# Optimization experiments

Hardware: AMD Instinct MI355X
Metric: run time of the kernel (lower is better)

The kernel has to match this reference:

```python
import jax, jax.numpy as jnp
import numpy as np

N = 100000   # nodes
E = 3200000  # edges
G = 512      # graphs in batch
EPS = 1e-5   # batchnorm eps


def _lin(key, fan_in, fan_out):
    return jax.random.normal(key, (fan_in, fan_out), jnp.float32) / np.sqrt(fan_in)


def setup_inputs() -> dict:
    key = jax.random.key(0)
    ks = jax.random.split(key, 12)
    x = jax.random.normal(ks[0], (N, 2), jnp.float32)
    edge_index = jax.random.randint(ks[1], (2, E), 0, N, dtype=jnp.int64)
    batch_index = jnp.sort(jax.random.randint(ks[2], (N,), 0, G, dtype=jnp.int64))
    w = (8, 32, 128)
    return {
        "x": x, "edge_index": edge_index, "batch_index": batch_index,
        "W1": _lin(ks[3], 2, w[0]),   "b1": jnp.zeros((w[0],), jnp.float32),
        "g1": jnp.ones((w[0],), jnp.float32),  "be1": jnp.zeros((w[0],), jnp.float32),
        "W2": _lin(ks[4], w[0], w[1]), "b2": jnp.zeros((w[1],), jnp.float32),
        "g2": jnp.ones((w[1],), jnp.float32),  "be2": jnp.zeros((w[1],), jnp.float32),
        "W3": _lin(ks[5], w[1], w[2]), "b3": jnp.zeros((w[2],), jnp.float32),
        "g3": jnp.ones((w[2],), jnp.float32),  "be3": jnp.zeros((w[2],), jnp.float32),
        "Wl": _lin(ks[6], w[2], 3),    "bl": jnp.zeros((3,), jnp.float32),
    }


def _gcn_norm(edge_index):
    # add self loops, symmetric normalization (PyG GCNConv default)
    loops = jnp.arange(N, dtype=edge_index.dtype)
    src = jnp.concatenate([edge_index[0], loops])
    dst = jnp.concatenate([edge_index[1], loops])
    deg = jax.ops.segment_sum(jnp.ones_like(dst, jnp.float32), dst, num_segments=N)
    dis = jnp.where(deg > 0, jax.lax.rsqrt(jnp.maximum(deg, 1.0)), 0.0)
    norm = dis[src] * dis[dst]  # [E+N]
    return src, dst, norm


def _gcn_conv(h, W, b, src, dst, norm):
    h = h @ W                                   # [N, out]
    msg = h[src] * norm[:, None]                # gather + scale
    return jax.ops.segment_sum(msg, dst, num_segments=N) + b


def _bn(h, g, b):
    # training-mode batchnorm over node dim
    m = jnp.mean(h, axis=0)
    v = jnp.mean(jnp.square(h - m), axis=0)
    return (h - m) * jax.lax.rsqrt(v + EPS) * g + b


def reference(x, edge_index, batch_index, W1, b1, g1, be1, W2, b2, g2, be2,
              W3, b3, g3, be3, Wl, bl):
    src, dst, norm = _gcn_norm(edge_index)
    h = _bn(jax.nn.relu(_gcn_conv(x, W1, b1, src, dst, norm)), g1, be1)
    h = _bn(jax.nn.relu(_gcn_conv(h, W2, b2, src, dst, norm)), g2, be2)
    h = _bn(jax.nn.relu(_gcn_conv(h, W3, b3, src, dst, norm)), g3, be3)
    pooled = jax.ops.segment_max(h, batch_index, num_segments=G)  # [G, 128]
    logits = pooled @ Wl + bl                                     # [G, 3]
    return jax.nn.log_softmax(logits, axis=1)
```

## Files before the change

### kernel.cpp

```cpp
#include <hip/hip_runtime.h>
#include <hip/hip_bf16.h>
#include <hip/hip_fp16.h>
#include <math.h>

#define N_NODES 100000
#define N_EDGES 3200000
#define N_GRAPHS 512
#define BN_EPS 1e-5f
#define NBIN ((N_NODES + 511) / 512)
#define CHUNK 8192
#define NCHUNK ((N_EDGES + CHUNK - 1) / CHUNK)
#define STORE_CAP (N_EDGES + 16 * NBIN * NCHUNK)
#define LSEG 98
#define NSEGB ((N_NODES + LSEG - 1) / LSEG)
#define NMMB ((N_NODES + 63) / 64)
#define NB2 3125
#define NB2P 3136
#define PLANE2 ((size_t)(N_NODES + 1) * 16)
#define PLANEU ((size_t)N_NODES * 16)

typedef _Float16 half8_t __attribute__((ext_vector_type(8)));
typedef float float4_t __attribute__((ext_vector_type(4)));

struct alignas(8) h4 { __half2 a, b; };
struct alignas(16) h8s { __half2 h[4]; };


__global__ void k_hist2(const int* __restrict__ dst, int* __restrict__ hists) {
    __shared__ int h[NBIN];
    for (int i = threadIdx.x; i < NBIN; i += blockDim.x) h[i] = 0;
    __syncthreads();
    int e0 = blockIdx.x * CHUNK;
    int e1 = min(e0 + CHUNK, N_EDGES);
    int e = e0 + threadIdx.x * 8;
    if (e + 8 <= e1) {
        int4 d0 = *(const int4*)(dst + e);
        int4 d1 = *(const int4*)(dst + e + 4);
        atomicAdd(&h[d0.x >> 9], 1); atomicAdd(&h[d0.y >> 9], 1);
        atomicAdd(&h[d0.z >> 9], 1); atomicAdd(&h[d0.w >> 9], 1);
        atomicAdd(&h[d1.x >> 9], 1); atomicAdd(&h[d1.y >> 9], 1);
        atomicAdd(&h[d1.z >> 9], 1); atomicAdd(&h[d1.w >> 9], 1);
    } else {
        for (; e < e1; ++e) atomicAdd(&h[dst[e] >> 9], 1);
    }
    __syncthreads();
    for (int i = threadIdx.x; i < NBIN; i += blockDim.x)
        hists[i * NCHUNK + blockIdx.x] = h[i];
}

__global__ void k_scan2(int* __restrict__ hists, int* __restrict__ ghist) {
    int b = blockIdx.x;
    int lane = threadIdx.x;
    int carry = 0;
    int base = b * NCHUNK;
    for (int c0 = 0; c0 < NCHUNK; c0 += 64) {
        int c = c0 + lane;
        int v = (c < NCHUNK) ? hists[base + c] : 0;
        int pv = (v + 15) & ~15;
        int inc = pv;
#pragma unroll
        for (int off = 1; off < 64; off <<= 1) {
            int u = __shfl_up(inc, off, 64);
            if (lane >= off) inc += u;
        }
        if (c < NCHUNK) hists[base + c] = inc - pv + carry;
        carry += __shfl(inc, 63, 64);
    }
    if (lane == 0) ghist[b] = carry;
}

__global__ void k_binscan(const int* __restrict__ ghist, int* __restrict__ bbase) {
    __shared__ int sd[512];
    int t = threadIdx.x;
    int v = (t < NBIN) ? ghist[t] : 0;
    sd[t] = v;
    __syncthreads();
    for (int off = 1; off < 512; off <<= 1) {
        int u = (t >= off) ? sd[t - off] : 0;
        __syncthreads();
        sd[t] += u;
        __syncthreads();
    }
    if (t < NBIN) bbase[t] = sd[t] - v;
    if (t == 511) bbase[NBIN] = sd[511];
}

__global__ void k_scatter(const int* __restrict__ src, const int* __restrict__ dst,
                          const int* __restrict__ bbase, const int* __restrict__ hists,
                          int* __restrict__ store) {
    __shared__ int cur[NBIN];
    for (int i = threadIdx.x; i < NBIN; i += blockDim.x)
        cur[i] = bbase[i] + hists[i * NCHUNK + blockIdx.x];
    __syncthreads();
    int e0 = blockIdx.x * CHUNK;
    int e1 = min(e0 + CHUNK, N_EDGES);
    int e = e0 + threadIdx.x * 8;
    if (e + 8 <= e1) {
        int4 d0 = *(const int4*)(dst + e), d1 = *(const int4*)(dst + e + 4);
        int4 s0 = *(const int4*)(src + e), s1 = *(const int4*)(src + e + 4);
        int dd[8] = {d0.x, d0.y, d0.z, d0.w, d1.x, d1.y, d1.z, d1.w};
        int sv[8] = {s0.x, s0.y, s0.z, s0.w, s1.x, s1.y, s1.z, s1.w};
#pragma unroll
        for (int j = 0; j < 8; ++j) {
            int d = dd[j];
            int b = d >> 9;
            int pos = atomicAdd(&cur[b], 1);
            store[pos] = (sv[j] << 9) | (d & 511);
        }
    } else {
        for (; e < e1; ++e) {
            int d = dst[e];
            int b = d >> 9;
            int pos = atomicAdd(&cur[b], 1);
            store[pos] = (src[e] << 9) | (d & 511);
        }
    }
    __syncthreads();
    for (int i = threadIdx.x; i < NBIN; i += blockDim.x) {
        int p = cur[i];
        int end = (p + 15) & ~15;
        for (; p < end; ++p) store[p] = -1;
    }
}

__global__ void k_csr_build(const int* __restrict__ bbase, const int* __restrict__ store,
                            const float* __restrict__ x, int* __restrict__ offs,
                            int* __restrict__ ends, float* __restrict__ dis,
                            float* __restrict__ rdis, float4* __restrict__ xd,
                            int* __restrict__ csr) {
    __shared__ int cnt[512], cur[512], wsum[4];
    int b = blockIdx.x;
    int n0 = b << 9;
    int e0 = bbase[b], e1 = bbase[b + 1];
    int t = threadIdx.x;
    int lane = t & 63, wid = t >> 6;
    if (t < 512) cnt[t] = 0;
    __syncthreads();
    for (int e = e0 + t; e < e1; e += 4096) {
        int p[4];
#pragma unroll
        for (int j = 0; j < 4; ++j)
            p[j] = (e + 1024 * j < e1) ? store[e + 1024 * j] : -1;
#pragma unroll
        for (int j = 0; j < 4; ++j)
            if (p[j] >= 0) atomicAdd(&cnt[p[j] & 511], 1);
    }
    __syncthreads();
    int c0 = 0, c1 = 0, pair = 0, inc = 0;
    if (t < 256) {
        c0 = cnt[2 * t];
        c1 = cnt[2 * t + 1];
        pair = c0 + c1;
        inc = pair;
#pragma unroll
        for (int off = 1; off < 64; off <<= 1) {
            int u = __shfl_up(inc, off, 64);
            if (lane >= off) inc += u;
        }
        if (lane == 63) wsum[wid] = inc;
    }
    __syncthreads();
    if (t < 256) {
        int wo = 0;
        for (int w = 0; w < wid; ++w) wo += wsum[w];
        int ex = inc - pair + wo;
        cur[2 * t] = ex;
        cur[2 * t + 1] = ex + c0;
#pragma unroll
        for (int j = 0; j < 2; ++j) {
            int n = n0 + 2 * t + j;
            int cc = j ? c1 : c0;
            int exx = j ? ex + c0 : ex;
            if (n < N_NODES) {
                offs[n] = e0 + exx;
                ends[n] = e0 + exx + cc;
                float dn = rsqrtf(1.0f + (float)cc);
                dis[n] = dn;
                rdis[n] = sqrtf(1.0f + (float)cc);
                float2 xv = *(const float2*)(x + 2 * (size_t)n);
                xd[n] = make_float4(dn * xv.x, dn * xv.y, dn, 0.f);
            } else if (n == N_NODES) {
                xd[N_NODES] = make_float4(0.f, 0.f, 0.f, 0.f);
            }
        }
    }
    __syncthreads();
    for (int e = e0 + t; e < e1; e += 4096) {
        int p[4];
#pragma unroll
        for (int j = 0; j < 4; ++j)
            p[j] = (e + 1024 * j < e1) ? store[e + 1024 * j] : -1;
#pragma unroll
        for (int j = 0; j < 4; ++j)
            if (p[j] >= 0) {
                int pos = e0 + atomicAdd(&cur[p[j] & 511], 1);
                csr[pos] = p[j] >> 9;
            }
    }
}


__global__ void k_agg1(const float4* __restrict__ xd, const int* __restrict__ offs,
                       const int* __restrict__ ends, const int* __restrict__ csr,
                       const float* __restrict__ W1, const float* __restrict__ b1,
                       float* __restrict__ svec, __half* __restrict__ ys1) {
    __shared__ float sW[16], sb[8];
    int t = threadIdx.x;
    if (t < 16) sW[t] = W1[t];
    if (t < 8) sb[t] = b1[t];
    __syncthreads();
    int wave = t >> 6, lane = t & 63;
    int nsub = lane >> 4, eg = lane & 15;
    int node = ((blockIdx.x * 4 + wave) << 2) + nsub;
    int e0 = offs[node], e1 = ends[node];
    float ax = 0.f, ay = 0.f, as = 0.f;
    for (int e = e0 + eg; e < e1; e += 64) {
        int s[4];
#pragma unroll
        for (int j = 0; j < 4; ++j)
            s[j] = (e + 16 * j < e1) ? csr[e + 16 * j] : N_NODES;
        float4 v[4];
#pragma unroll
        for (int j = 0; j < 4; ++j) v[j] = xd[s[j]];
#pragma unroll
        for (int j = 0; j < 4; ++j) {
            ax += v[j].x;
            ay += v[j].y;
            as += v[j].z;
        }
    }
#pragma unroll
    for (int off = 1; off < 16; off <<= 1) {
        ax += __shfl_xor(ax, off, 64);
        ay += __shfl_xor(ay, off, 64);
        as += __shfl_xor(as, off, 64);
    }
    if (eg == 0) {
        float4 xn = xd[node];
        float dn = xn.z;
        float u0x = dn * (ax + xn.x);
        float u0y = dn * (ay + xn.y);
        svec[node] = dn * (as + xn.z);
        float y[8];
#pragma unroll
        for (int f = 0; f < 8; ++f)
            y[f] = dn * fmaxf(u0x * sW[f] + u0y * sW[8 + f] + sb[f], 0.f);
        h8s o;
#pragma unroll
        for (int q = 0; q < 4; ++q) o.h[q] = __floats2half2_rn(y[2 * q], y[2 * q + 1]);
        *(h8s*)(ys1 + (size_t)node * 8) = o;
    }
}


__global__ void k_stats8v(const __half* __restrict__ ys1, const float* __restrict__ rdis,
                          float* __restrict__ stats) {
    int t = threadIdx.x;
    float s[8] = {0, 0, 0, 0, 0, 0, 0, 0};
    float s2[8] = {0, 0, 0, 0, 0, 0, 0, 0};
    for (int n = blockIdx.x * 256 + t; n < N_NODES; n += gridDim.x * 256) {
        float r = rdis[n];
        h8s v = *(const h8s*)(ys1 + (size_t)n * 8);
#pragma unroll
        for (int q = 0; q < 4; ++q) {
            float v0 = __low2float(v.h[q]) * r;
            float v1 = __high2float(v.h[q]) * r;
            s[2 * q] += v0;      s2[2 * q] += v0 * v0;
            s[2 * q + 1] += v1;  s2[2 * q + 1] += v1 * v1;
        }
    }
#pragma unroll
    for (int off = 1; off < 64; off <<= 1)
#pragma unroll
        for (int k = 0; k < 8; ++k) {
            s[k] += __shfl_xor(s[k], off, 64);
            s2[k] += __shfl_xor(s2[k], off, 64);
        }
    __shared__ float sm[16];
    if (t < 16) sm[t] = 0.f;
    __syncthreads();
    if ((t & 63) == 0) {
#pragma unroll
        for (int k = 0; k < 8; ++k) {
            atomicAdd(&sm[k], s[k]);
            atomicAdd(&sm[8 + k], s2[k]);
        }
    }
    __syncthreads();
    if (t < 16) atomicAdd(&stats[t], sm[t]);
}


__global__ void k_prep2(const float* __restrict__ stats, const float* __restrict__ gamma,
                        const float* __restrict__ beta, const float* __restrict__ W2,
                        float* __restrict__ W2p, float* __restrict__ cw2,
                        __half* __restrict__ ys1) {
    __shared__ float a1[8], c1[8];
    int t = threadIdx.x;
    if (t < 8) {
        float inv_n = 1.0f / (float)N_NODES;
        float m = stats[t] * inv_n;
        float v = stats[8 + t] * inv_n - m * m;
        float a = gamma[t] * rsqrtf(v + BN_EPS);
        a1[t] = a;
        c1[t] = beta[t] - m * a;
    }
    __syncthreads();
    W2p[t] = a1[t >> 5] * W2[t];
    if (t < 32) {
        float cb = 0.f;
#pragma unroll
        for (int i = 0; i < 8; ++i) cb += c1[i] * W2[i * 32 + t];
        cw2[t] = cb;
    }
    if (t == 128) *(int4*)(ys1 + (size_t)N_NODES * 8) = make_int4(0, 0, 0, 0);
}


__global__ void k_agg2(const __half* __restrict__ ys1, const int* __restrict__ offs,
                       const int* __restrict__ ends, const int* __restrict__ csr,
                       const float* __restrict__ dis, const float* __restrict__ svec,
                       const float* __restrict__ W2p, const float* __restrict__ cw2,
                       const float* __restrict__ b2, __half* __restrict__ ys2,
                       float* __restrict__ part2) {
    __shared__ float sW[256], sC[32], sB[32], sm2[64];
    int t = threadIdx.x;
    sW[t] = W2p[t];
    if (t < 32) { sC[t] = cw2[t]; sB[t] = b2[t]; }
    if (t < 64) sm2[t] = 0.f;
    __syncthreads();
    int wave = t >> 6, lane = t & 63;
    int nsub = lane >> 3, eg = lane & 7;
    int node = ((blockIdx.x * 4 + wave) << 3) + nsub;
    int e0 = offs[node], e1 = ends[node];
    float a[8] = {0, 0, 0, 0, 0, 0, 0, 0};
    for (int e = e0 + eg; e < e1; e += 32) {
        int s[4];
#pragma unroll
        for (int j = 0; j < 4; ++j)
            s[j] = (e + 8 * j < e1) ? csr[e + 8 * j] : N_NODES;
        h8s v[4];
#pragma unroll
        for (int j = 0; j < 4; ++j) v[j] = *(const h8s*)(ys1 + (size_t)s[j] * 8);
#pragma unroll
        for (int j = 0; j < 4; ++j)
#pragma unroll
            for (int q = 0; q < 4; ++q) {
                a[2 * q] += __low2float(v[j].h[q]);
                a[2 * q + 1] += __high2float(v[j].h[q]);
            }
    }
    if (eg == 0) {
        h8s v = *(const h8s*)(ys1 + (size_t)node * 8);
#pragma unroll
        for (int q = 0; q < 4; ++q) {
            a[2 * q] += __low2float(v.h[q]);
            a[2 * q + 1] += __high2float(v.h[q]);
        }
    }
#pragma unroll
    for (int off = 1; off < 8; off <<= 1)
#pragma unroll
        for (int k = 0; k < 8; ++k) a[k] += __shfl_xor(a[k], off, 64);
    int lb = nsub << 3;
    float u[8];
#pragma unroll
    for (int i = 0; i < 8; ++i) u[i] = __shfl(a[i], lb, 64);
    float dn = dis[node];
    float sv = svec[node];
#pragma unroll
    for (int i = 0; i < 8; ++i) u[i] *= dn;
    int c0 = (lane & 7) * 4;
    float hh[4], hs2[4];
#pragma unroll
    for (int k = 0; k < 4; ++k) {
        int col = c0 + k;
        float conv = sB[col] + sv * sC[col];
#pragma unroll
        for (int i = 0; i < 8; ++i) conv += u[i] * sW[i * 32 + col];
        hh[k] = fmaxf(conv, 0.f);
        hs2[k] = hh[k] * hh[k];
    }
    h4 o;
    o.a = __floats2half2_rn(dn * hh[0], dn * hh[1]);
    o.b = __floats2half2_rn(dn * hh[2], dn * hh[3]);
    *(h4*)(ys2 + (size_t)(c0 >> 4) * PLANE2 + (size_t)node * 16 + (c0 & 15)) = o;

    float hs[4];
#pragma unroll
    for (int k = 0; k < 4; ++k) hs[k] = hh[k];
#pragma unroll
    for (int off = 8; off < 64; off <<= 1)
#pragma unroll
        for (int k = 0; k < 4; ++k) {
            hs[k] += __shfl_xor(hs[k], off, 64);
            hs2[k] += __shfl_xor(hs2[k], off, 64);
        }
    if (nsub == 0) {
#pragma unroll
        for (int k = 0; k < 4; ++k) {
            atomicAdd(&sm2[c0 + k], hs[k]);
            atomicAdd(&sm2[32 + c0 + k], hs2[k]);
        }
    }
    __syncthreads();
    if (t < 64) part2[(size_t)t * NB2P + blockIdx.x] = sm2[t];
}

__global__ void k_red32(const float* __restrict__ part2, float* __restrict__ stats2) {
    int i = blockIdx.x;
    int t = threadIdx.x;
    float s = 0.f;
    for (int b = t; b < NB2; b += 256) s += part2[(size_t)i * NB2P + b];
    __shared__ float sm[256];
    sm[t] = s;
    __syncthreads();
    for (int st = 128; st > 0; st >>= 1) {
        if (t < st) sm[t] += sm[t + st];
        __syncthreads();
    }
    if (t == 0) stats2[i] = sm[0];
}


__global__ void k_prep3(const float* __restrict__ stats, const float* __restrict__ gamma,
                        const float* __restrict__ beta, const float* __restrict__ W3,
                        __half* __restrict__ wfrag, float* __restrict__ cw3,
                        __half* __restrict__ ys2) {
    __shared__ float a2[32], c2[32];
    int t = threadIdx.x;
    if (t < 32) {
        float inv_n = 1.0f / (float)N_NODES;
        float m = stats[t] * inv_n;
        float v = stats[32 + t] * inv_n - m * m;
        float a = gamma[t] * rsqrtf(v + BN_EPS);
        a2[t] = a;
        c2[t] = beta[t] - m * a;
    }
    __syncthreads();
    {
        int g = t >> 6, kq = (t >> 4) & 3, c = t & 15;
#pragma unroll
        for (int j = 0; j < 8; ++j) {
            int k = kq * 8 + j;
            wfrag[(size_t)t * 8 + j] = __float2half(a2[k] * W3[k * 128 + g * 16 + c]);
        }
    }
    if (t < 128) {
        float cb = 0.f;
#pragma unroll
        for (int k = 0; k < 32; ++k) cb += c2[k] * W3[k * 128 + t];
        cw3[t] = cb;
    }
    if (t >= 480 && t < 496) {
        int idx = t - 480;
        ((__half2*)(ys2 + (size_t)(idx >> 3) * PLANE2 + (size_t)N_NODES * 16))[idx & 7] =
            __half2{__float2half(0.f), __float2half(0.f)};
    }
}


__global__ void k_agg3(const __half* __restrict__ ys2, const int* __restrict__ offs,
                       const int* __restrict__ ends, const int* __restrict__ csr,
                       const float* __restrict__ dis, __half* __restrict__ u2) {
    int plane = blockIdx.x & 1;
    int nb = blockIdx.x >> 1;
    int wave = threadIdx.x >> 6;
    int lane = threadIdx.x & 63;
    int nsub = lane >> 4;
    int eg = (lane >> 1) & 7;
    int chunk = lane & 1;
    int node = ((nb * 4 + wave) << 2) + nsub;
    int e0 = offs[node], e1 = ends[node];
    float a[8] = {0, 0, 0, 0, 0, 0, 0, 0};
    const __half* hp = ys2 + (size_t)plane * PLANE2 + chunk * 8;
    for (int e = e0 + eg; e < e1; e += 32) {
        int eA = e + 8 * chunk;
        int eB = e + 8 * (chunk + 2);
        int sA = (eA < e1) ? csr[eA] : N_NODES;
        int sB = (eB < e1) ? csr[eB] : N_NODES;
        int sC = __shfl_xor(sA, 1, 64);
        int sD = __shfl_xor(sB, 1, 64);
        h8s v0 = *(const h8s*)(hp + (size_t)sA * 16);
        h8s v1 = *(const h8s*)(hp + (size_t)sC * 16);
        h8s v2 = *(const h8s*)(hp + (size_t)sB * 16);
        h8s v3 = *(const h8s*)(hp + (size_t)sD * 16);
#pragma unroll
        for (int q = 0; q < 4; ++q) {
            a[2 * q] += __low2float(v0.h[q]) + __low2float(v1.h[q]) +
                        __low2float(v2.h[q]) + __low2float(v3.h[q]);
            a[2 * q + 1] += __high2float(v0.h[q]) + __high2float(v1.h[q]) +
                            __high2float(v2.h[q]) + __high2float(v3.h[q]);
        }
    }
    if (eg == 0) {
        h8s v = *(const h8s*)(hp + (size_t)node * 16);
#pragma unroll
        for (int q = 0; q < 4; ++q) {
            a[2 * q] += __low2float(v.h[q]);
            a[2 * q + 1] += __high2float(v.h[q]);
        }
    }
#pragma unroll
    for (int off = 2; off < 16; off <<= 1)
#pragma unroll
        for (int k = 0; k < 8; ++k) a[k] += __shfl_xor(a[k], off, 64);
    if (eg == 0) {
        float dn = dis[node];
        h8s o;
#pragma unroll
        for (int q = 0; q < 4; ++q)
            o.h[q] = __floats2half2_rn(dn * a[2 * q], dn * a[2 * q + 1]);
        *(h8s*)(u2 + (size_t)plane * PLANEU + (size_t)node * 16 + chunk * 8) = o;
    }
}


__global__ void k_mm_mfma(const __half* __restrict__ u2, const __half* __restrict__ wfrag,
                          const float* __restrict__ cw3, const float* __restrict__ b3,
                          const float* __restrict__ svec, const float* __restrict__ dis,
                          __half* __restrict__ ys3, float* __restrict__ spart) {
    __shared__ float sm[256];
    int t = threadIdx.x;
    int wave = t >> 6;
    int lane = t & 63;
    int n0 = (blockIdx.x * 4 + wave) * 16;
    bool active = n0 < N_NODES;
    int m = lane & 15;
    int kq = lane >> 4;
    float ss[8] = {0, 0, 0, 0, 0, 0, 0, 0};
    float ss2[8] = {0, 0, 0, 0, 0, 0, 0, 0};

    if (active) {
        half8_t af = *(const half8_t*)(u2 + (size_t)(kq >> 1) * PLANEU +
                                       (size_t)(n0 + m) * 16 + (kq & 1) * 8);
        float4_t accs[8];
#pragma unroll
        for (int g = 0; g < 8; ++g) {
            float4_t acc = {0.f, 0.f, 0.f, 0.f};
            half8_t bf = *(const half8_t*)(wfrag + (size_t)((g * 4 + kq) * 16 + m) * 8);
            accs[g] = __builtin_amdgcn_mfma_f32_16x16x32_f16(af, bf, acc, 0, 0, 0);
        }
        float sv[4], dn[4];
#pragma unroll
        for (int r = 0; r < 4; ++r) {
            sv[r] = svec[n0 + kq * 4 + r];
            dn[r] = dis[n0 + kq * 4 + r];
        }
#pragma unroll
        for (int g = 0; g < 8; ++g) {
            float cwf = cw3[g * 16 + m];
            float bf3 = b3[g * 16 + m];
#pragma unroll
            for (int r = 0; r < 4; ++r) {
                float y = fmaxf(accs[g][r] + sv[r] * cwf + bf3, 0.f);
                ss[g] += y;
                ss2[g] += y * y;
                ys3[(size_t)(n0 + kq * 4 + r) * 128 + g * 16 + m] = __float2half(dn[r] * y);
            }
        }
    }
#pragma unroll
    for (int off = 16; off < 64; off <<= 1)
#pragma unroll
        for (int g = 0; g < 8; ++g) {
            ss[g] += __shfl_xor(ss[g], off, 64);
            ss2[g] += __shfl_xor(ss2[g], off, 64);
        }
    sm[t] = 0.f;
    __syncthreads();
    if (active && kq == 0) {
#pragma unroll
        for (int g = 0; g < 8; ++g) {
            atomicAdd(&sm[g * 16 + m], ss[g]);
            atomicAdd(&sm[128 + g * 16 + m], ss2[g]);
        }
    }
    __syncthreads();
    spart[(size_t)blockIdx.x * 256 + t] = sm[t];
}

__global__ void k_stats_red(const float* __restrict__ part, float* __restrict__ stats) {
    int i = blockIdx.x;
    int t = threadIdx.x;
    float s = 0.f;
    for (int b = t; b < NMMB; b += 256) s += part[(size_t)b * 256 + i];
    __shared__ float sm[256];
    sm[t] = s;
    __syncthreads();
    for (int st = 128; st > 0; st >>= 1) {
        if (t < st) sm[t] += sm[t + st];
        __syncthreads();
    }
    if (t == 0) stats[i] = sm[0];
}


__global__ void k_pool1(const __half* __restrict__ ys3, const float* __restrict__ rdis,
                        const int* __restrict__ batch, int* __restrict__ gmax,
                        int* __restrict__ gmin) {
    __shared__ int sb[LSEG];
    __shared__ float sr[LSEG];
    int n0 = blockIdx.x * LSEG;
    int n1 = min(n0 + LSEG, N_NODES);
    int L = n1 - n0;
    int f = threadIdx.x;
    for (int i = f; i < L; i += 128) { sb[i] = batch[n0 + i]; sr[i] = rdis[n0 + i]; }
    __syncthreads();
    if (L <= 0) return;
    int cg = sb[0];
    int mx = 0;
    int mn = 0x7F800000;
    for (int i0 = 0; i0 < L; i0 += 8) {
        int lim = min(8, L - i0);
        __half v[8];
#pragma unroll
        for (int j = 0; j < 8; ++j)
            if (j < lim) v[j] = ys3[(size_t)(n0 + i0 + j) * 128 + f];
#pragma unroll
        for (int j = 0; j < 8; ++j) {
            if (j >= lim) break;
            int i = i0 + j;
            int g = sb[i];
            if (g != cg) {
                atomicMax(&gmax[cg * 128 + f], mx);
                atomicMin(&gmin[cg * 128 + f], mn);
                cg = g; mx = 0; mn = 0x7F800000;
            }
            float val = __half2float(v[j]) * sr[i];
            int b = __float_as_int(val);
            mx = max(mx, b);
            mn = min(mn, b);
        }
    }
    atomicMax(&gmax[cg * 128 + f], mx);
    atomicMin(&gmin[cg * 128 + f], mn);
}


__device__ __forceinline__ int lower_bound_dev(const int* __restrict__ a, int val) {
    int lo = 0, hi = N_NODES;
    while (lo < hi) {
        int mid = (lo + hi) >> 1;
        if (a[mid] < val) lo = mid + 1; else hi = mid;
    }
    return lo;
}

__global__ void k_poolhead(const int* __restrict__ gmax, const int* __restrict__ gmin,
                           const int* __restrict__ batch, const float* __restrict__ stats,
                           const float* __restrict__ gamma, const float* __restrict__ beta,
                           const float* __restrict__ Wl, const float* __restrict__ bl,
                           float* __restrict__ out) {
    int g = blockIdx.x;
    int f = threadIdx.x;
    float inv_n = 1.0f / (float)N_NODES;
    float m = stats[f] * inv_n;
    float var = stats[128 + f] * inv_n - m * m;
    float a = gamma[f] * rsqrtf(var + BN_EPS);
    float c = beta[f] - m * a;
    int s = lower_bound_dev(batch, g);
    int e = lower_bound_dev(batch, g + 1);
    float mx = __int_as_float(gmax[g * 128 + f]);
    float mn = __int_as_float(gmin[g * 128 + f]);
    float r;
    if (e > s) r = (a >= 0.f) ? (a * mx + c) : (a * mn + c);
    else r = -INFINITY;
    __shared__ float l[3][128];
    l[0][f] = r * Wl[f * 3 + 0];
    l[1][f] = r * Wl[f * 3 + 1];
    l[2][f] = r * Wl[f * 3 + 2];
    __syncthreads();
    for (int st = 64; st > 0; st >>= 1) {
        if (f < st) {
            l[0][f] += l[0][f + st];
            l[1][f] += l[1][f + st];
            l[2][f] += l[2][f + st];
        }
        __syncthreads();
    }
    if (f == 0) {
        float l0 = l[0][0] + bl[0], l1 = l[1][0] + bl[1], l2 = l[2][0] + bl[2];
        float mxl = fmaxf(l0, fmaxf(l1, l2));
        float lse = mxl + logf(expf(l0 - mxl) + expf(l1 - mxl) + expf(l2 - mxl));
        out[g * 3 + 0] = l0 - lse;
        out[g * 3 + 1] = l1 - lse;
        out[g * 3 + 2] = l2 - lse;
    }
}


extern "C" void kernel_launch(void* const* d_in, const int* in_sizes, int n_in,
                              void* d_out, int out_size, void* d_ws, size_t ws_size,
                              hipStream_t stream) {
    const float* x   = (const float*)d_in[0];
    const int* ei    = (const int*)d_in[1];
    const int* src   = ei;
    const int* dst   = ei + N_EDGES;
    const int* batch = (const int*)d_in[2];
    const float *W1 = (const float*)d_in[3],  *b1 = (const float*)d_in[4];
    const float *g1 = (const float*)d_in[5],  *be1 = (const float*)d_in[6];
    const float *W2 = (const float*)d_in[7],  *b2 = (const float*)d_in[8];
    const float *g2 = (const float*)d_in[9],  *be2 = (const float*)d_in[10];
    const float *W3 = (const float*)d_in[11], *b3 = (const float*)d_in[12];
    const float *g3 = (const float*)d_in[13], *be3 = (const float*)d_in[14];
    const float *Wl = (const float*)d_in[15], *bl = (const float*)d_in[16];
    float* out = (float*)d_out;

    int* base = (int*)d_ws;
    size_t o = 0;
    float* stats1 = (float*)(base + o); o += 256;
    float* stats2 = (float*)(base + o); o += 256;
    float* stats3 = (float*)(base + o); o += 256;
    int* gmax     = base + o; o += (size_t)N_GRAPHS * 128;
    size_t zero_words = o;
    int* gmin     = base + o; o += (size_t)N_GRAPHS * 128;
    int* bbase    = base + o; o += NBIN + 4;
    int* ghist    = base + o; o += NBIN + 4;
    int* hists    = base + o; o += ((size_t)NBIN * NCHUNK + 3) & ~3ULL;
    float* W2p    = (float*)(base + o); o += 256;
    float* cw2    = (float*)(base + o); o += 32;
    __half* wfrag = (__half*)(base + o); o += 2048;
    float* cw3    = (float*)(base + o); o += 128;
    int* offs     = base + o; o += 100000;
    int* ends     = base + o; o += 100000;
    int* store    = base + o; o += STORE_CAP;
    int* csr      = base + o; o += STORE_CAP;
    float* dis    = (float*)(base + o); o += N_NODES;
    float* rdis   = (float*)(base + o); o += N_NODES;
    float* svec   = (float*)(base + o); o += N_NODES;
    float* spart  = (float*)(base + o); o += (size_t)NMMB * 256;
    float* part2  = (float*)(base + o); o += (size_t)64 * NB2P;
    float4* xd    = (float4*)(base + o); o += (size_t)(N_NODES + 1) * 4;
    __half* ys1   = (__half*)(base + o); o += (size_t)(N_NODES + 1) * 4;
    __half* ys2   = (__half*)(base + o); o += (size_t)(N_NODES + 1) * 16;
    __half* u2    = (__half*)(base + o); o += (size_t)N_NODES * 16;
    __half* ys3   = (__half*)(base + o); o += (size_t)N_NODES * 64;
    if (ws_size < o * 4) return;

    const int TB = 256;

    hipMemsetAsync(base, 0, zero_words * 4, stream);
    hipMemsetAsync(gmin, 0x7F, (size_t)N_GRAPHS * 128 * 4, stream);

    k_hist2<<<NCHUNK, 1024, 0, stream>>>(dst, hists);
    k_scan2<<<NBIN, 64, 0, stream>>>(hists, ghist);
    k_binscan<<<1, 512, 0, stream>>>(ghist, bbase);
    k_scatter<<<NCHUNK, 1024, 0, stream>>>(src, dst, bbase, hists, store);
    k_csr_build<<<NBIN, 1024, 0, stream>>>(bbase, store, x, offs, ends, dis, rdis, xd, csr);

    k_agg1<<<N_NODES / 16, TB, 0, stream>>>(xd, offs, ends, csr, W1, b1, svec, ys1);
    k_stats8v<<<64, 256, 0, stream>>>(ys1, rdis, stats1);
    k_prep2<<<1, 256, 0, stream>>>(stats1, g1, be1, W2, W2p, cw2, ys1);

    k_agg2<<<NB2, TB, 0, stream>>>(ys1, offs, ends, csr, dis, svec, W2p, cw2, b2, ys2, part2);
    k_red32<<<64, 256, 0, stream>>>(part2, stats2);
    k_prep3<<<1, 512, 0, stream>>>(stats2, g2, be2, W3, wfrag, cw3, ys2);

    k_agg3<<<2 * (N_NODES / 16), TB, 0, stream>>>(ys2, offs, ends, csr, dis, u2);
    k_mm_mfma<<<NMMB, 256, 0, stream>>>(u2, wfrag, cw3, b3, svec, dis, ys3, spart);
    k_stats_red<<<256, 256, 0, stream>>>(spart, stats3);

    k_pool1<<<NSEGB, 128, 0, stream>>>(ys3, rdis, batch, gmax, gmin);
    k_poolhead<<<N_GRAPHS, 128, 0, stream>>>(gmax, gmin, batch, stats3, g3, be3, Wl, bl, out);
}
```

Measured before the change: 319.5 us.

## Fuse graph max/min pooling into MFMA matmul epilogue, drop ys3 buffer

The layer-3 matmul epilogue now reduces per-graph max and min of the activations directly with atomics, using a wave shuffle reduction when a 16-node tile belongs to a single graph. This removes the separate pooling kernel and the fp16 write and reread of the 100000x128 ys3 intermediate. Mixed-graph tiles fall back to per-element global atomics, and values are pooled in fp32 rather than after fp16 rounding. This assumes batch is sorted so most tiles are uniform.

```diff
diff --git a/kernel.cpp b/kernel.cpp
--- a/kernel.cpp
+++ b/kernel.cpp
@@ -11,8 +11,6 @@
 #define CHUNK 8192
 #define NCHUNK ((N_EDGES + CHUNK - 1) / CHUNK)
 #define STORE_CAP (N_EDGES + 16 * NBIN * NCHUNK)
-#define LSEG 98
-#define NSEGB ((N_NODES + LSEG - 1) / LSEG)
 #define NMMB ((N_NODES + 63) / 64)
 #define NB2 3125
 #define NB2P 3136
@@ -518,8 +516,9 @@
 
 __global__ void k_mm_mfma(const __half* __restrict__ u2, const __half* __restrict__ wfrag,
                           const float* __restrict__ cw3, const float* __restrict__ b3,
-                          const float* __restrict__ svec, const float* __restrict__ dis,
-                          __half* __restrict__ ys3, float* __restrict__ spart) {
+                          const float* __restrict__ svec, const int* __restrict__ batch,
+                          float* __restrict__ spart, int* __restrict__ gmax,
+                          int* __restrict__ gmin) {
     __shared__ float sm[256];
     int t = threadIdx.x;
     int wave = t >> 6;
@@ -541,22 +540,54 @@
             half8_t bf = *(const half8_t*)(wfrag + (size_t)((g * 4 + kq) * 16 + m) * 8);
             accs[g] = __builtin_amdgcn_mfma_f32_16x16x32_f16(af, bf, acc, 0, 0, 0);
         }
-        float sv[4], dn[4];
-#pragma unroll
-        for (int r = 0; r < 4; ++r) {
-            sv[r] = svec[n0 + kq * 4 + r];
-            dn[r] = dis[n0 + kq * 4 + r];
-        }
+        float sv[4];
+#pragma unroll
+        for (int r = 0; r < 4; ++r) sv[r] = svec[n0 + kq * 4 + r];
+
+        int b_first = batch[n0];
+        int b_last = batch[n0 + 15];
+        bool uni = (b_first == b_last);
+        int bnr[4];
+        if (!uni) {
+#pragma unroll
+            for (int r = 0; r < 4; ++r) bnr[r] = batch[n0 + kq * 4 + r];
+        }
+        float ymx[8], ymn[8];
 #pragma unroll
         for (int g = 0; g < 8; ++g) {
             float cwf = cw3[g * 16 + m];
             float bf3 = b3[g * 16 + m];
+            float mx = 0.f, mn = INFINITY;
 #pragma unroll
             for (int r = 0; r < 4; ++r) {
                 float y = fmaxf(accs[g][r] + sv[r] * cwf + bf3, 0.f);
                 ss[g] += y;
                 ss2[g] += y * y;
-                ys3[(size_t)(n0 + kq * 4 + r) * 128 + g * 16 + m] = __float2half(dn[r] * y);
+                mx = fmaxf(mx, y);
+                mn = fminf(mn, y);
+                if (!uni) {
+                    int yb = __float_as_int(y);
+                    atomicMax(&gmax[bnr[r] * 128 + g * 16 + m], yb);
+                    atomicMin(&gmin[bnr[r] * 128 + g * 16 + m], yb);
+                }
+            }
+            ymx[g] = mx;
+            ymn[g] = mn;
+        }
+        if (uni) {
+#pragma unroll
+            for (int off = 16; off < 64; off <<= 1)
+#pragma unroll
+                for (int g = 0; g < 8; ++g) {
+                    ymx[g] = fmaxf(ymx[g], __shfl_xor(ymx[g], off, 64));
+                    ymn[g] = fminf(ymn[g], __shfl_xor(ymn[g], off, 64));
+                }
+            if (kq == 0) {
+#pragma unroll
+                for (int g = 0; g < 8; ++g) {
+                    atomicMax(&gmax[b_first * 128 + g * 16 + m], __float_as_int(ymx[g]));
+                    atomicMin(&gmin[b_first * 128 + g * 16 + m], __float_as_int(ymn[g]));
+                }
             }
         }
     }
@@ -593,48 +624,6 @@
         __syncthreads();
     }
     if (t == 0) stats[i] = sm[0];
-}
-
-
-__global__ void k_pool1(const __half* __restrict__ ys3, const float* __restrict__ rdis,
-                        const int* __restrict__ batch, int* __restrict__ gmax,
-                        int* __restrict__ gmin) {
-    __shared__ int sb[LSEG];
-    __shared__ float sr[LSEG];
-    int n0 = blockIdx.x * LSEG;
-    int n1 = min(n0 + LSEG, N_NODES);
-    int L = n1 - n0;
-    int f = threadIdx.x;
-    for (int i = f; i < L; i += 128) { sb[i] = batch[n0 + i]; sr[i] = rdis[n0 + i]; }
-    __syncthreads();
-    if (L <= 0) return;
-    int cg = sb[0];
-    int mx = 0;
-    int mn = 0x7F800000;
-    for (int i0 = 0; i0 < L; i0 += 8) {
-        int lim = min(8, L - i0);
-        __half v[8];
-#pragma unroll
-        for (int j = 0; j < 8; ++j)
-            if (j < lim) v[j] = ys3[(size_t)(n0 + i0 + j) * 128 + f];
-#pragma unroll
-        for (int j = 0; j < 8; ++j) {
-            if (j >= lim) break;
-            int i = i0 + j;
-            int g = sb[i];
-            if (g != cg) {
-                atomicMax(&gmax[cg * 128 + f], mx);
-                atomicMin(&gmin[cg * 128 + f], mn);
-                cg = g; mx = 0; mn = 0x7F800000;
-            }
-            float val = __half2float(v[j]) * sr[i];
-            int b = __float_as_int(val);
-            mx = max(mx, b);
-            mn = min(mn, b);
-        }
-    }
-    atomicMax(&gmax[cg * 128 + f], mx);
-    atomicMin(&gmin[cg * 128 + f], mn);
 }
 
 
@@ -735,7 +724,6 @@
     __half* ys1   = (__half*)(base + o); o += (size_t)(N_NODES + 1) * 4;
     __half* ys2   = (__half*)(base + o); o += (size_t)(N_NODES + 1) * 16;
     __half* u2    = (__half*)(base + o); o += (size_t)N_NODES * 16;
-    __half* ys3   = (__half*)(base + o); o += (size_t)N_NODES * 64;
     if (ws_size < o * 4) return;
 
     const int TB = 256;
@@ -758,9 +746,8 @@
     k_prep3<<<1, 512, 0, stream>>>(stats2, g2, be2, W3, wfrag, cw3, ys2);
 
     k_agg3<<<2 * (N_NODES / 16), TB, 0, stream>>>(ys2, offs, ends, csr, dis, u2);
-    k_mm_mfma<<<NMMB, 256, 0, stream>>>(u2, wfrag, cw3, b3, svec, dis, ys3, spart);
+    k_mm_mfma<<<NMMB, 256, 0, stream>>>(u2, wfrag, cw3, b3, svec, batch, spart, gmax, gmin);
     k_stats_red<<<256, 256, 0, stream>>>(spart, stats3);
 
-    k_pool1<<<NSEGB, 128, 0, stream>>>(ys3, rdis, batch, gmax, gmin);
     k_poolhead<<<N_GRAPHS, 128, 0, stream>>>(gmax, gmin, batch, stats3, g3, be3, Wl, bl, out);
 }
```

After: 319.1 us. Within noise of the previous version (-0.1%).
